# Kernel tuning notes

Hardware: AMD Instinct MI355X
Metric: run time of the kernel (lower is better)

The kernel has to match this reference:

```python
import jax, jax.numpy as jnp
import numpy as np

N = 50000
E = 800000


def gcn_conv(x, W, b, src, dst, norm):
    # x: [N, Fin] -> [N, Fout]; PyG GCNConv: linear, normalized scatter-add, bias
    h = x @ W                                  # [N, Fout]
    msg = h[src] * norm[:, None]               # [E+N, Fout] gather + scale
    out = jax.ops.segment_sum(msg, dst, num_segments=N)  # scatter-add
    return out + b


def _with_self_loops(edge_index):
    loops = jnp.arange(N, dtype=edge_index.dtype)
    src = jnp.concatenate([edge_index[0], loops])
    dst = jnp.concatenate([edge_index[1], loops])
    return src, dst


def _gcn_norm(src, dst):
    deg = jax.ops.segment_sum(jnp.ones_like(src, dtype=jnp.float32), dst, num_segments=N)
    dinv = jnp.where(deg > 0, jax.lax.rsqrt(jnp.maximum(deg, 1.0)), 0.0)
    return dinv[src] * dinv[dst]


def setup_inputs() -> dict:
    key = jax.random.key(0)
    ks = jax.random.split(key, 8)
    x = jax.random.normal(ks[0], (N, 128), dtype=jnp.float32)
    edge_index = jax.random.randint(ks[1], (2, E), 0, N, dtype=jnp.int64)
    # Glorot-ish init for the three GCNConv layers
    W1 = jax.random.normal(ks[2], (128, 64), dtype=jnp.float32) * (1.0 / np.sqrt(128))
    b1 = jnp.zeros((64,), dtype=jnp.float32)
    W2 = jax.random.normal(ks[3], (64, 64), dtype=jnp.float32) * (1.0 / np.sqrt(64))
    b2 = jnp.zeros((64,), dtype=jnp.float32)
    W3 = jax.random.normal(ks[4], (64, 40), dtype=jnp.float32) * (1.0 / np.sqrt(64))
    b3 = jnp.zeros((40,), dtype=jnp.float32)
    return {"x": x, "edge_index": edge_index, "W1": W1, "b1": b1,
            "W2": W2, "b2": b2, "W3": W3, "b3": b3}


def reference(x, edge_index, W1, b1, W2, b2, W3, b3):
    src, dst = _with_self_loops(edge_index)
    norm = _gcn_norm(src, dst)
    h = jax.nn.relu(gcn_conv(x, W1, b1, src, dst, norm))
    h = jax.nn.relu(gcn_conv(h, W2, b2, src, dst, norm))
    return gcn_conv(h, W3, b3, src, dst, norm)
```

## Files before the change

### kernel.cpp

```cpp
#include <hip/hip_runtime.h>

#define NNODE 50000
#define NEDGE 800000
#define NBUCKET 196
#define NPB 256
#define EPB 3125

typedef __attribute__((ext_vector_type(8))) unsigned short ushort8v;

__device__ inline unsigned short f2bf(float f) {
    unsigned int u = __float_as_uint(f);
    u += 0x7FFFu + ((u >> 16) & 1u);
    return (unsigned short)(u >> 16);
}
__device__ inline float bf2f(unsigned short h) {
    return __uint_as_float((unsigned int)h << 16);
}


__global__ __launch_bounds__(256) void k_histA(const int* __restrict__ dst, int* __restrict__ hist_g) {
    __shared__ int h[NBUCKET];
    const int tid = threadIdx.x, pb = blockIdx.x, e0 = pb * EPB;
    if (tid < NBUCKET) h[tid] = 0;
    __syncthreads();
    for (int i = tid; i < EPB; i += 256)
        atomicAdd(&h[dst[e0 + i] >> 8], 1);
    __syncthreads();
    if (tid < NBUCKET) hist_g[tid * 256 + pb] = h[tid];
}

__global__ __launch_bounds__(256) void k_scanA1(const int* __restrict__ hist_g, int* __restrict__ base_g,
                                                int* __restrict__ colsum) {
    __shared__ int s[256];
    const int b = blockIdx.x, t = threadIdx.x;
    int v = hist_g[b * 256 + t];
    s[t] = v;
    __syncthreads();
#pragma unroll
    for (int off = 1; off < 256; off <<= 1) {
        int a = (t >= off) ? s[t - off] : 0;
        __syncthreads();
        s[t] += a;
        __syncthreads();
    }
    base_g[b * 256 + t] = s[t] - v;
    if (t == 255) colsum[b] = s[t];
}

__device__ inline void scan_colsum(const int* __restrict__ colsum, int* cs, int tid) {
    cs[tid] = (tid < NBUCKET) ? colsum[tid] : 0;
    __syncthreads();
#pragma unroll
    for (int off = 1; off < 256; off <<= 1) {
        int a = (tid >= off) ? cs[tid - off] : 0;
        __syncthreads();
        cs[tid] += a;
        __syncthreads();
    }
}

__global__ __launch_bounds__(256) void k_scatterA(const int* __restrict__ src, const int* __restrict__ dst,
                          const int* __restrict__ base_g, const int* __restrict__ colsum,
                          unsigned int* __restrict__ bucketed) {
    __shared__ int cs[256];
    __shared__ int cur[NBUCKET];
    const int tid = threadIdx.x, pb = blockIdx.x, e0 = pb * EPB;
    scan_colsum(colsum, cs, tid);
    if (tid < NBUCKET) {
        int bb = (tid == 0) ? 0 : cs[tid - 1];
        cur[tid] = bb + base_g[tid * 256 + pb];
    }
    __syncthreads();
    for (int i = tid; i < EPB; i += 256) {
        int d = dst[e0 + i], s = src[e0 + i];
        int pos = atomicAdd(&cur[d >> 8], 1);
        bucketed[pos] = ((unsigned int)d << 16) | (unsigned int)s;
    }
}


__global__ __launch_bounds__(256) void k_bucketB2(const unsigned int* __restrict__ bucketed,
                          const int* __restrict__ colsum, int* __restrict__ rowstart,
                          unsigned short* __restrict__ csr_src, float* __restrict__ dinv) {
    __shared__ int cs[256];
    __shared__ int cnt[NPB];
    __shared__ int ex[NPB];
    __shared__ int cur[NPB];
    const int tid = threadIdx.x, b = blockIdx.x;
    scan_colsum(colsum, cs, tid);
    const int base_out = (b == 0) ? 0 : cs[b - 1];
    const int end_out  = cs[b];

    cnt[tid] = 0;
    __syncthreads();
    for (int i = base_out + tid; i < end_out; i += 256)
        atomicAdd(&cnt[(bucketed[i] >> 16) & 255], 1);
    __syncthreads();

    int v = cnt[tid];
    ex[tid] = v;
    __syncthreads();
#pragma unroll
    for (int off = 1; off < 256; off <<= 1) {
        int a = (tid >= off) ? ex[tid - off] : 0;
        __syncthreads();
        ex[tid] += a;
        __syncthreads();
    }
    int excl = ex[tid] - v;
    int node = (b << 8) + tid;
    cur[tid] = base_out + excl;
    if (node < NNODE) {
        rowstart[node] = base_out + excl;
        dinv[node] = rsqrtf((float)v + 1.0f);
    }
    if (b == 0 && tid == 0) rowstart[NNODE] = NEDGE;
    __syncthreads();

    for (int i = base_out + tid; i < end_out; i += 256) {
        unsigned int u = bucketed[i];
        int pos = atomicAdd(&cur[(u >> 16) & 255], 1);
        csr_src[pos] = (unsigned short)(u & 0xFFFFu);
    }
}


template<int FIN, int FOUT, typename XT>
__launch_bounds__(256)
__global__ void k_gemm_prescale(const XT* __restrict__ X, const float* __restrict__ W,
                                const float* __restrict__ dinv, unsigned short* __restrict__ XWs) {
    __shared__ float Xt[FIN * 68];
    __shared__ float Ws[FIN * 64];

    const int tid = threadIdx.x;
    const int r0 = blockIdx.x * 64;

    for (int idx = tid; idx < FIN * 64; idx += 256) {
        int k = idx >> 6, c = idx & 63;
        Ws[idx] = (c < FOUT) ? W[k * FOUT + c] : 0.0f;
    }

    if constexpr (sizeof(XT) == 4) {
        constexpr int CH = FIN / 4;
        constexpr int CSH = (FIN == 128) ? 5 : 4;
        for (int idx = tid; idx < 64 * CH; idx += 256) {
            int r_lo = idx & 7;
            int c = (idx >> 3) & (CH - 1);
            int r = ((idx >> (3 + CSH)) << 3) + r_lo;
            int rr = r0 + r; if (rr >= NNODE) rr = NNODE - 1;
            float4 v = *(const float4*)((const float*)X + (size_t)rr * FIN + c * 4);
            Xt[(4 * c + 0) * 68 + r] = v.x;
            Xt[(4 * c + 1) * 68 + r] = v.y;
            Xt[(4 * c + 2) * 68 + r] = v.z;
            Xt[(4 * c + 3) * 68 + r] = v.w;
        }
    } else {
        constexpr int CH = FIN / 8;
        constexpr int CSH = (FIN == 128) ? 4 : 3;
        for (int idx = tid; idx < 64 * CH; idx += 256) {
            int r_lo = idx & 7;
            int c = (idx >> 3) & (CH - 1);
            int r = ((idx >> (3 + CSH)) << 3) + r_lo;
            int rr = r0 + r; if (rr >= NNODE) rr = NNODE - 1;
            ushort8v v = *(const ushort8v*)((const unsigned short*)X + (size_t)rr * FIN + c * 8);
#pragma unroll
            for (int t = 0; t < 8; ++t)
                Xt[(8 * c + t) * 68 + r] = bf2f(v[t]);
        }
    }
    __syncthreads();

    const int cg = tid & 15;
    const int rg = tid >> 4;

    float acc[4][4] = {};
#pragma unroll 4
    for (int k = 0; k < FIN; ++k) {
        float4 xv = *(const float4*)&Xt[k * 68 + 4 * rg];
        float4 wv = *(const float4*)&Ws[k * 64 + 4 * cg];
#pragma unroll
        for (int i = 0; i < 4; ++i) {
            float xi = (i == 0) ? xv.x : (i == 1) ? xv.y : (i == 2) ? xv.z : xv.w;
            acc[i][0] = fmaf(xi, wv.x, acc[i][0]);
            acc[i][1] = fmaf(xi, wv.y, acc[i][1]);
            acc[i][2] = fmaf(xi, wv.z, acc[i][2]);
            acc[i][3] = fmaf(xi, wv.w, acc[i][3]);
        }
    }

    if (4 * cg + 4 <= FOUT) {
#pragma unroll
        for (int i = 0; i < 4; ++i) {
            int row = r0 + 4 * rg + i;
            if (row < NNODE) {
                float dv = dinv[row];
                ushort4 o = { f2bf(acc[i][0] * dv), f2bf(acc[i][1] * dv),
                              f2bf(acc[i][2] * dv), f2bf(acc[i][3] * dv) };
                *(ushort4*)(XWs + (size_t)row * FOUT + 4 * cg) = o;
            }
        }
    }
}


template<int F, bool RELU, bool OUTBF>
__launch_bounds__(256)
__global__ void k_aggregate(const unsigned short* __restrict__ XWs, const int* __restrict__ rowstart,
                            const unsigned short* __restrict__ csr_src, const float* __restrict__ dinv,
                            const float* __restrict__ b, void* __restrict__ outp) {
    constexpr int NQ = F / 8;
    const int wid  = threadIdx.x >> 6;
    const int lane = threadIdx.x & 63;
    const int g = lane >> 3;
    const int q = lane & 7;
    const int d = blockIdx.x * 4 + wid;
    if (d >= NNODE) return;

    const int beg = rowstart[d];
    const int end = rowstart[d + 1];
    const bool qa = (q < NQ);

    float acc[8] = {};

    for (int base = beg; base < end; base += 64) {
        int idx = base + lane;
        int sv = (idx < end) ? (int)csr_src[idx] : 0;
        int nv = min(64, end - base);
        for (int j = 0; j < nv; j += 8) {
            int jj = j + g;
            int s = __shfl(sv, jj);
            if (jj < nv && qa) {
                ushort8v v = *(const ushort8v*)(XWs + (size_t)s * F + 8 * q);
#pragma unroll
                for (int t = 0; t < 8; ++t) acc[t] += bf2f(v[t]);
            }
        }
    }

#pragma unroll
    for (int mask = 8; mask <= 32; mask <<= 1) {
#pragma unroll
        for (int t = 0; t < 8; ++t) acc[t] += __shfl_xor(acc[t], mask);
    }

    if (g == 0 && qa) {
        ushort8v self = *(const ushort8v*)(XWs + (size_t)d * F + 8 * q);
        float dv = dinv[d];
        float o[8];
#pragma unroll
        for (int t = 0; t < 8; ++t) {
            o[t] = fmaf(acc[t] + bf2f(self[t]), dv, b[8 * q + t]);
            if (RELU) o[t] = fmaxf(o[t], 0.f);
        }
        if (OUTBF) {
            ushort8v ov;
#pragma unroll
            for (int t = 0; t < 8; ++t) ov[t] = f2bf(o[t]);
            *(ushort8v*)((unsigned short*)outp + (size_t)d * F + 8 * q) = ov;
        } else {
            float4 o0 = { o[0], o[1], o[2], o[3] };
            float4 o1 = { o[4], o[5], o[6], o[7] };
            *(float4*)((float*)outp + (size_t)d * F + 8 * q)     = o0;
            *(float4*)((float*)outp + (size_t)d * F + 8 * q + 4) = o1;
        }
    }
}

extern "C" void kernel_launch(void* const* d_in, const int* in_sizes, int n_in,
                              void* d_out, int out_size, void* d_ws, size_t ws_size,
                              hipStream_t stream) {
    const float* x  = (const float*)d_in[0];
    const int*   ei = (const int*)d_in[1];
    const float* W1 = (const float*)d_in[2];
    const float* b1 = (const float*)d_in[3];
    const float* W2 = (const float*)d_in[4];
    const float* b2 = (const float*)d_in[5];
    const float* W3 = (const float*)d_in[6];
    const float* b3 = (const float*)d_in[7];
    float* out = (float*)d_out;

    const int* src = ei;
    const int* dst = ei + NEDGE;

    char* p = (char*)d_ws;
    auto alloc = [&](size_t bytes) { char* r = p; p += (bytes + 255) & ~size_t(255); return r; };
    unsigned int* bucketed = (unsigned int*)alloc((size_t)NEDGE * 4);
    int*   hist_g     = (int*)  alloc(NBUCKET * 256 * 4);
    int*   base_g     = (int*)  alloc(NBUCKET * 256 * 4);
    int*   colsum     = (int*)  alloc(NBUCKET * 4);
    int*   rowstart   = (int*)  alloc((NNODE + 1) * 4);
    unsigned short* csr_src = (unsigned short*)alloc((size_t)NEDGE * 2);
    float* dinv       = (float*)alloc(NNODE * 4);
    unsigned short* XWs = (unsigned short*)alloc((size_t)NNODE * 64 * 2 + 256);
    unsigned short* H1  = (unsigned short*)alloc((size_t)NNODE * 64 * 2 + 256);
    unsigned short* H2  = (unsigned short*)alloc((size_t)NNODE * 64 * 2 + 256);

    const int B = 256;
    const int gGemm = (NNODE + 63) / 64;
    const int gAgg  = (NNODE + 3) / 4;

    k_histA   <<<256, B, 0, stream>>>(dst, hist_g);
    k_scanA1  <<<NBUCKET, B, 0, stream>>>(hist_g, base_g, colsum);
    k_scatterA<<<256, B, 0, stream>>>(src, dst, base_g, colsum, bucketed);
    k_bucketB2<<<NBUCKET, B, 0, stream>>>(bucketed, colsum, rowstart, csr_src, dinv);

    k_gemm_prescale<128, 64, float><<<gGemm, B, 0, stream>>>(x, W1, dinv, XWs);
    k_aggregate<64, true, true><<<gAgg, B, 0, stream>>>(XWs, rowstart, csr_src, dinv, b1, H1);

    k_gemm_prescale<64, 64, unsigned short><<<gGemm, B, 0, stream>>>(H1, W2, dinv, XWs);
    k_aggregate<64, true, true><<<gAgg, B, 0, stream>>>(XWs, rowstart, csr_src, dinv, b2, H2);

    k_gemm_prescale<64, 40, unsigned short><<<gGemm, B, 0, stream>>>(H2, W3, dinv, XWs);
    k_aggregate<40, false, false><<<gAgg, B, 0, stream>>>(XWs, rowstart, csr_src, dinv, b3, out);
}
```

Baseline: 158.1 us.

## Fuse CSR build into one cooperative kernel with grid syncs; unpack bf16 via uint4

The four CSR-construction kernels (histogram, column scan, scatter into buckets, per-bucket sort) are merged into a single cooperative kernel. It runs on 242 blocks and uses grid.sync() between phases, removing three kernel launch boundaries. The chunk size changes so the edges fit in 242 blocks, and the scan now masks hist columns beyond CHUNKS. The aggregation kernel also loads neighbour rows as uint4 and unpacks bf16 pairs with shift/mask instead of a ushort8 vector. The cooperative launch requires all blocks to be co-resident, and grid syncs have their own cost.

```diff
diff --git a/kernel.cpp b/kernel.cpp
--- a/kernel.cpp
+++ b/kernel.cpp
@@ -1,10 +1,12 @@
 #include <hip/hip_runtime.h>
+#include <hip/hip_cooperative_groups.h>
 
 #define NNODE 50000
 #define NEDGE 800000
 #define NBUCKET 196
 #define NPB 256
-#define EPB 3125
+#define CHUNKS 242
+#define CEPB 3306
 
 typedef __attribute__((ext_vector_type(8))) unsigned short ushort8v;
 
@@ -16,111 +18,113 @@
 __device__ inline float bf2f(unsigned short h) {
     return __uint_as_float((unsigned int)h << 16);
 }
-
-
-__global__ __launch_bounds__(256) void k_histA(const int* __restrict__ dst, int* __restrict__ hist_g) {
-    __shared__ int h[NBUCKET];
-    const int tid = threadIdx.x, pb = blockIdx.x, e0 = pb * EPB;
-    if (tid < NBUCKET) h[tid] = 0;
-    __syncthreads();
-    for (int i = tid; i < EPB; i += 256)
-        atomicAdd(&h[dst[e0 + i] >> 8], 1);
-    __syncthreads();
-    if (tid < NBUCKET) hist_g[tid * 256 + pb] = h[tid];
-}
-
-__global__ __launch_bounds__(256) void k_scanA1(const int* __restrict__ hist_g, int* __restrict__ base_g,
-                                                int* __restrict__ colsum) {
-    __shared__ int s[256];
-    const int b = blockIdx.x, t = threadIdx.x;
-    int v = hist_g[b * 256 + t];
-    s[t] = v;
-    __syncthreads();
-#pragma unroll
-    for (int off = 1; off < 256; off <<= 1) {
-        int a = (t >= off) ? s[t - off] : 0;
-        __syncthreads();
-        s[t] += a;
-        __syncthreads();
-    }
-    base_g[b * 256 + t] = s[t] - v;
-    if (t == 255) colsum[b] = s[t];
-}
-
-__device__ inline void scan_colsum(const int* __restrict__ colsum, int* cs, int tid) {
-    cs[tid] = (tid < NBUCKET) ? colsum[tid] : 0;
-    __syncthreads();
-#pragma unroll
-    for (int off = 1; off < 256; off <<= 1) {
-        int a = (tid >= off) ? cs[tid - off] : 0;
-        __syncthreads();
-        cs[tid] += a;
-        __syncthreads();
-    }
-}
-
-__global__ __launch_bounds__(256) void k_scatterA(const int* __restrict__ src, const int* __restrict__ dst,
-                          const int* __restrict__ base_g, const int* __restrict__ colsum,
-                          unsigned int* __restrict__ bucketed) {
-    __shared__ int cs[256];
-    __shared__ int cur[NBUCKET];
-    const int tid = threadIdx.x, pb = blockIdx.x, e0 = pb * EPB;
-    scan_colsum(colsum, cs, tid);
-    if (tid < NBUCKET) {
-        int bb = (tid == 0) ? 0 : cs[tid - 1];
-        cur[tid] = bb + base_g[tid * 256 + pb];
-    }
-    __syncthreads();
-    for (int i = tid; i < EPB; i += 256) {
-        int d = dst[e0 + i], s = src[e0 + i];
-        int pos = atomicAdd(&cur[d >> 8], 1);
-        bucketed[pos] = ((unsigned int)d << 16) | (unsigned int)s;
-    }
-}
-
-
-__global__ __launch_bounds__(256) void k_bucketB2(const unsigned int* __restrict__ bucketed,
-                          const int* __restrict__ colsum, int* __restrict__ rowstart,
-                          unsigned short* __restrict__ csr_src, float* __restrict__ dinv) {
-    __shared__ int cs[256];
-    __shared__ int cnt[NPB];
-    __shared__ int ex[NPB];
-    __shared__ int cur[NPB];
-    const int tid = threadIdx.x, b = blockIdx.x;
-    scan_colsum(colsum, cs, tid);
-    const int base_out = (b == 0) ? 0 : cs[b - 1];
-    const int end_out  = cs[b];
-
-    cnt[tid] = 0;
-    __syncthreads();
-    for (int i = base_out + tid; i < end_out; i += 256)
-        atomicAdd(&cnt[(bucketed[i] >> 16) & 255], 1);
-    __syncthreads();
-
-    int v = cnt[tid];
-    ex[tid] = v;
-    __syncthreads();
-#pragma unroll
-    for (int off = 1; off < 256; off <<= 1) {
-        int a = (tid >= off) ? ex[tid - off] : 0;
-        __syncthreads();
-        ex[tid] += a;
-        __syncthreads();
-    }
-    int excl = ex[tid] - v;
-    int node = (b << 8) + tid;
-    cur[tid] = base_out + excl;
-    if (node < NNODE) {
-        rowstart[node] = base_out + excl;
-        dinv[node] = rsqrtf((float)v + 1.0f);
-    }
-    if (b == 0 && tid == 0) rowstart[NNODE] = NEDGE;
-    __syncthreads();
-
-    for (int i = base_out + tid; i < end_out; i += 256) {
-        unsigned int u = bucketed[i];
-        int pos = atomicAdd(&cur[(u >> 16) & 255], 1);
-        csr_src[pos] = (unsigned short)(u & 0xFFFFu);
+__device__ inline float bfLO(unsigned int u) { return __uint_as_float(u << 16); }
+__device__ inline float bfHI(unsigned int u) { return __uint_as_float(u & 0xFFFF0000u); }
+
+
+__global__ __launch_bounds__(256)
+void k_csr(const int* __restrict__ src, const int* __restrict__ dst,
+           int* __restrict__ hist_g, int* __restrict__ base_g, int* __restrict__ colsum,
+           unsigned int* __restrict__ bucketed, int* __restrict__ rowstart,
+           unsigned short* __restrict__ csr_src, float* __restrict__ dinv) {
+    cooperative_groups::grid_group grid = cooperative_groups::this_grid();
+    __shared__ int sA[256];
+    __shared__ int sB[256];
+    __shared__ int sC[256];
+    const int tid = threadIdx.x, bid = blockIdx.x;
+
+    {
+        const int e0 = bid * CEPB, e1 = min(e0 + CEPB, NEDGE);
+        if (tid < NBUCKET) sA[tid] = 0;
+        __syncthreads();
+        for (int i = e0 + tid; i < e1; i += 256) atomicAdd(&sA[dst[i] >> 8], 1);
+        __syncthreads();
+        if (tid < NBUCKET) hist_g[tid * 256 + bid] = sA[tid];
+    }
+    grid.sync();
+
+    if (bid < NBUCKET) {
+        int v = (tid < CHUNKS) ? hist_g[bid * 256 + tid] : 0;
+        sA[tid] = v;
+        __syncthreads();
+#pragma unroll
+        for (int off = 1; off < 256; off <<= 1) {
+            int a = (tid >= off) ? sA[tid - off] : 0;
+            __syncthreads();
+            sA[tid] += a;
+            __syncthreads();
+        }
+        base_g[bid * 256 + tid] = sA[tid] - v;
+        if (tid == 255) colsum[bid] = sA[255];
+    }
+    grid.sync();
+
+    {
+        sA[tid] = (tid < NBUCKET) ? colsum[tid] : 0;
+        __syncthreads();
+#pragma unroll
+        for (int off = 1; off < 256; off <<= 1) {
+            int a = (tid >= off) ? sA[tid - off] : 0;
+            __syncthreads();
+            sA[tid] += a;
+            __syncthreads();
+        }
+        if (tid < NBUCKET) {
+            int bb = (tid == 0) ? 0 : sA[tid - 1];
+            sB[tid] = bb + base_g[tid * 256 + bid];
+        }
+        __syncthreads();
+        const int e0 = bid * CEPB, e1 = min(e0 + CEPB, NEDGE);
+        for (int i = e0 + tid; i < e1; i += 256) {
+            int d = dst[i], s = src[i];
+            int pos = atomicAdd(&sB[d >> 8], 1);
+            bucketed[pos] = ((unsigned int)d << 16) | (unsigned int)s;
+        }
+    }
+    grid.sync();
+
+    if (bid < NBUCKET) {
+        sA[tid] = (tid < NBUCKET) ? colsum[tid] : 0;
+        __syncthreads();
+#pragma unroll
+        for (int off = 1; off < 256; off <<= 1) {
+            int a = (tid >= off) ? sA[tid - off] : 0;
+            __syncthreads();
+            sA[tid] += a;
+            __syncthreads();
+        }
+        const int base_out = (bid == 0) ? 0 : sA[bid - 1];
+        const int end_out  = sA[bid];
+        __syncthreads();
+        sB[tid] = 0;
+        __syncthreads();
+        for (int i = base_out + tid; i < end_out; i += 256)
+            atomicAdd(&sB[(bucketed[i] >> 16) & 255], 1);
+        __syncthreads();
+        int v = sB[tid];
+        sC[tid] = v;
+        __syncthreads();
+#pragma unroll
+        for (int off = 1; off < 256; off <<= 1) {
+            int a = (tid >= off) ? sC[tid - off] : 0;
+            __syncthreads();
+            sC[tid] += a;
+            __syncthreads();
+        }
+        int excl = sC[tid] - v;
+        int node = (bid << 8) + tid;
+        sB[tid] = base_out + excl;
+        if (node < NNODE) {
+            rowstart[node] = base_out + excl;
+            dinv[node] = rsqrtf((float)v + 1.0f);
+        }
+        if (bid == 0 && tid == 0) rowstart[NNODE] = NEDGE;
+        __syncthreads();
+        for (int i = base_out + tid; i < end_out; i += 256) {
+            unsigned int u = bucketed[i];
+            int pos = atomicAdd(&sB[(u >> 16) & 255], 1);
+            csr_src[pos] = (unsigned short)(u & 0xFFFFu);
+        }
     }
 }
 
@@ -230,9 +234,11 @@
             int jj = j + g;
             int s = __shfl(sv, jj);
             if (jj < nv && qa) {
-                ushort8v v = *(const ushort8v*)(XWs + (size_t)s * F + 8 * q);
-#pragma unroll
-                for (int t = 0; t < 8; ++t) acc[t] += bf2f(v[t]);
+                uint4 v = *(const uint4*)(XWs + (size_t)s * F + 8 * q);
+                acc[0] += bfLO(v.x); acc[1] += bfHI(v.x);
+                acc[2] += bfLO(v.y); acc[3] += bfHI(v.y);
+                acc[4] += bfLO(v.z); acc[5] += bfHI(v.z);
+                acc[6] += bfLO(v.w); acc[7] += bfHI(v.w);
             }
         }
     }
@@ -244,12 +250,14 @@
     }
 
     if (g == 0 && qa) {
-        ushort8v self = *(const ushort8v*)(XWs + (size_t)d * F + 8 * q);
+        uint4 sv4 = *(const uint4*)(XWs + (size_t)d * F + 8 * q);
+        float self[8] = { bfLO(sv4.x), bfHI(sv4.x), bfLO(sv4.y), bfHI(sv4.y),
+                          bfLO(sv4.z), bfHI(sv4.z), bfLO(sv4.w), bfHI(sv4.w) };
         float dv = dinv[d];
         float o[8];
 #pragma unroll
         for (int t = 0; t < 8; ++t) {
-            o[t] = fmaf(acc[t] + bf2f(self[t]), dv, b[8 * q + t]);
+            o[t] = fmaf(acc[t] + self[t], dv, b[8 * q + t]);
             if (RELU) o[t] = fmaxf(o[t], 0.f);
         }
         if (OUTBF) {
@@ -290,7 +298,7 @@
     int*   colsum     = (int*)  alloc(NBUCKET * 4);
     int*   rowstart   = (int*)  alloc((NNODE + 1) * 4);
     unsigned short* csr_src = (unsigned short*)alloc((size_t)NEDGE * 2);
-    float* dinv       = (float*)alloc(NNODE * 4);
+    float* dinvp      = (float*)alloc(NNODE * 4);
     unsigned short* XWs = (unsigned short*)alloc((size_t)NNODE * 64 * 2 + 256);
     unsigned short* H1  = (unsigned short*)alloc((size_t)NNODE * 64 * 2 + 256);
     unsigned short* H2  = (unsigned short*)alloc((size_t)NNODE * 64 * 2 + 256);
@@ -299,17 +307,17 @@
     const int gGemm = (NNODE + 63) / 64;
     const int gAgg  = (NNODE + 3) / 4;
 
-    k_histA   <<<256, B, 0, stream>>>(dst, hist_g);
-    k_scanA1  <<<NBUCKET, B, 0, stream>>>(hist_g, base_g, colsum);
-    k_scatterA<<<256, B, 0, stream>>>(src, dst, base_g, colsum, bucketed);
-    k_bucketB2<<<NBUCKET, B, 0, stream>>>(bucketed, colsum, rowstart, csr_src, dinv);
-
-    k_gemm_prescale<128, 64, float><<<gGemm, B, 0, stream>>>(x, W1, dinv, XWs);
-    k_aggregate<64, true, true><<<gAgg, B, 0, stream>>>(XWs, rowstart, csr_src, dinv, b1, H1);
-
-    k_gemm_prescale<64, 64, unsigned short><<<gGemm, B, 0, stream>>>(H1, W2, dinv, XWs);
-    k_aggregate<64, true, true><<<gAgg, B, 0, stream>>>(XWs, rowstart, csr_src, dinv, b2, H2);
-
-    k_gemm_prescale<64, 40, unsigned short><<<gGemm, B, 0, stream>>>(H2, W3, dinv, XWs);
-    k_aggregate<40, false, false><<<gAgg, B, 0, stream>>>(XWs, rowstart, csr_src, dinv, b3, out);
-}
+    void* args[] = { (void*)&src, (void*)&dst, (void*)&hist_g, (void*)&base_g,
+                     (void*)&colsum, (void*)&bucketed, (void*)&rowstart,
+                     (void*)&csr_src, (void*)&dinvp };
+    hipLaunchCooperativeKernel((const void*)k_csr, dim3(CHUNKS), dim3(B), args, 0, stream);
+
+    k_gemm_prescale<128, 64, float><<<gGemm, B, 0, stream>>>(x, W1, dinvp, XWs);
+    k_aggregate<64, true, true><<<gAgg, B, 0, stream>>>(XWs, rowstart, csr_src, dinvp, b1, H1);
+
+    k_gemm_prescale<64, 64, unsigned short><<<gGemm, B, 0, stream>>>(H1, W2, dinvp, XWs);
+    k_aggregate<64, true, true><<<gAgg, B, 0, stream>>>(XWs, rowstart, csr_src, dinvp, b2, H2);
+
+    k_gemm_prescale<64, 40, unsigned short><<<gGemm, B, 0, stream>>>(H2, W3, dinvp, XWs);
+    k_aggregate<40, false, false><<<gAgg, B, 0, stream>>>(XWs, rowstart, csr_src, dinvp, b3, out);
+}
```

Measured after the change: 259.1 us. 1.64x slower.

## Fuse aggregation with next layer's GEMM to skip hidden-state round trips

Applied to the files above, without the earlier changes.

Adds a k_agg_gemm kernel. Each block aggregates neighbor features for 64 nodes straight into shared memory, applies bias and ReLU, then multiplies by the next layer's weights and writes the dinv-prescaled bf16 result. This removes the bf16 H1/H2 global writes and reads and two kernel launches. As a side change, the bf16 unpack now reads uint4 and uses shift/mask helpers. The cost is that each block now runs the aggregation with only 4 wavefronts over 16 nodes each, with no gather overlap across separate kernels, which may lower parallelism in the latency-bound gather phase.

```diff
diff --git a/kernel.cpp b/kernel.cpp
--- a/kernel.cpp
+++ b/kernel.cpp
@@ -16,6 +16,8 @@
 __device__ inline float bf2f(unsigned short h) {
     return __uint_as_float((unsigned int)h << 16);
 }
+__device__ inline float bfLO(unsigned int u) { return __uint_as_float(u << 16); }
+__device__ inline float bfHI(unsigned int u) { return __uint_as_float(u & 0xFFFF0000u); }
 
 
 __global__ __launch_bounds__(256) void k_histA(const int* __restrict__ dst, int* __restrict__ hist_g) {
@@ -77,7 +79,6 @@
         bucketed[pos] = ((unsigned int)d << 16) | (unsigned int)s;
     }
 }
-
 
 __global__ __launch_bounds__(256) void k_bucketB2(const unsigned int* __restrict__ bucketed,
                           const int* __restrict__ colsum, int* __restrict__ rowstart,
@@ -125,9 +126,9 @@
 }
 
 
-template<int FIN, int FOUT, typename XT>
+template<int FIN, int FOUT>
 __launch_bounds__(256)
-__global__ void k_gemm_prescale(const XT* __restrict__ X, const float* __restrict__ W,
+__global__ void k_gemm_prescale(const float* __restrict__ X, const float* __restrict__ W,
                                 const float* __restrict__ dinv, unsigned short* __restrict__ XWs) {
     __shared__ float Xt[FIN * 68];
     __shared__ float Ws[FIN * 64];
@@ -140,33 +141,18 @@
         Ws[idx] = (c < FOUT) ? W[k * FOUT + c] : 0.0f;
     }
 
-    if constexpr (sizeof(XT) == 4) {
-        constexpr int CH = FIN / 4;
-        constexpr int CSH = (FIN == 128) ? 5 : 4;
-        for (int idx = tid; idx < 64 * CH; idx += 256) {
-            int r_lo = idx & 7;
-            int c = (idx >> 3) & (CH - 1);
-            int r = ((idx >> (3 + CSH)) << 3) + r_lo;
-            int rr = r0 + r; if (rr >= NNODE) rr = NNODE - 1;
-            float4 v = *(const float4*)((const float*)X + (size_t)rr * FIN + c * 4);
-            Xt[(4 * c + 0) * 68 + r] = v.x;
-            Xt[(4 * c + 1) * 68 + r] = v.y;
-            Xt[(4 * c + 2) * 68 + r] = v.z;
-            Xt[(4 * c + 3) * 68 + r] = v.w;
-        }
-    } else {
-        constexpr int CH = FIN / 8;
-        constexpr int CSH = (FIN == 128) ? 4 : 3;
-        for (int idx = tid; idx < 64 * CH; idx += 256) {
-            int r_lo = idx & 7;
-            int c = (idx >> 3) & (CH - 1);
-            int r = ((idx >> (3 + CSH)) << 3) + r_lo;
-            int rr = r0 + r; if (rr >= NNODE) rr = NNODE - 1;
-            ushort8v v = *(const ushort8v*)((const unsigned short*)X + (size_t)rr * FIN + c * 8);
-#pragma unroll
-            for (int t = 0; t < 8; ++t)
-                Xt[(8 * c + t) * 68 + r] = bf2f(v[t]);
-        }
+    constexpr int CH = FIN / 4;
+    constexpr int CSH = (FIN == 128) ? 5 : 4;
+    for (int idx = tid; idx < 64 * CH; idx += 256) {
+        int r_lo = idx & 7;
+        int c = (idx >> 3) & (CH - 1);
+        int r = ((idx >> (3 + CSH)) << 3) + r_lo;
+        int rr = r0 + r; if (rr >= NNODE) rr = NNODE - 1;
+        float4 v = *(const float4*)(X + (size_t)rr * FIN + c * 4);
+        Xt[(4 * c + 0) * 68 + r] = v.x;
+        Xt[(4 * c + 1) * 68 + r] = v.y;
+        Xt[(4 * c + 2) * 68 + r] = v.z;
+        Xt[(4 * c + 3) * 68 + r] = v.w;
     }
     __syncthreads();
 
@@ -203,11 +189,113 @@
 }
 
 
-template<int F, bool RELU, bool OUTBF>
+template<int FOUT>
+__launch_bounds__(256)
+__global__ void k_agg_gemm(const unsigned short* __restrict__ XWin, const int* __restrict__ rowstart,
+                           const unsigned short* __restrict__ csr_src, const float* __restrict__ dinv,
+                           const float* __restrict__ bias, const float* __restrict__ W,
+                           unsigned short* __restrict__ XWout) {
+    __shared__ float Xt[64 * 68];
+    __shared__ float Ws[64 * 64];
+
+    const int tid = threadIdx.x;
+    const int wid = tid >> 6, lane = tid & 63;
+    const int g = lane >> 3, q = lane & 7;
+    const int r0 = blockIdx.x * 64;
+
+    for (int idx = tid; idx < 64 * 64; idx += 256) {
+        int k = idx >> 6, c = idx & 63;
+        Ws[idx] = (c < FOUT) ? W[k * FOUT + c] : 0.0f;
+    }
+
+    float bb[8];
+#pragma unroll
+    for (int t = 0; t < 8; ++t) bb[t] = bias[8 * q + t];
+
+    for (int n = 0; n < 16; ++n) {
+        const int rr = wid * 16 + n;
+        const int d = r0 + rr;
+        if (d < NNODE) {
+            const int beg = rowstart[d];
+            const int end = rowstart[d + 1];
+            float acc[8] = {};
+            for (int base = beg; base < end; base += 64) {
+                int idx = base + lane;
+                int sv = (idx < end) ? (int)csr_src[idx] : 0;
+                int nv = min(64, end - base);
+                for (int j = 0; j < nv; j += 8) {
+                    int jj = j + g;
+                    int s = __shfl(sv, jj);
+                    if (jj < nv) {
+                        uint4 v = *(const uint4*)(XWin + (size_t)s * 64 + 8 * q);
+                        acc[0] += bfLO(v.x); acc[1] += bfHI(v.x);
+                        acc[2] += bfLO(v.y); acc[3] += bfHI(v.y);
+                        acc[4] += bfLO(v.z); acc[5] += bfHI(v.z);
+                        acc[6] += bfLO(v.w); acc[7] += bfHI(v.w);
+                    }
+                }
+            }
+#pragma unroll
+            for (int mask = 8; mask <= 32; mask <<= 1) {
+#pragma unroll
+                for (int t = 0; t < 8; ++t) acc[t] += __shfl_xor(acc[t], mask);
+            }
+            if (g == 0) {
+                uint4 sv4 = *(const uint4*)(XWin + (size_t)d * 64 + 8 * q);
+                float self[8] = { bfLO(sv4.x), bfHI(sv4.x), bfLO(sv4.y), bfHI(sv4.y),
+                                  bfLO(sv4.z), bfHI(sv4.z), bfLO(sv4.w), bfHI(sv4.w) };
+                float dv = dinv[d];
+#pragma unroll
+                for (int t = 0; t < 8; ++t) {
+                    float o = fmaf(acc[t] + self[t], dv, bb[t]);
+                    Xt[(8 * q + t) * 68 + rr] = fmaxf(o, 0.0f);
+                }
+            }
+        } else if (g == 0) {
+#pragma unroll
+            for (int t = 0; t < 8; ++t) Xt[(8 * q + t) * 68 + rr] = 0.0f;
+        }
+    }
+    __syncthreads();
+
+    const int cg = tid & 15;
+    const int rg = tid >> 4;
+
+    float acc[4][4] = {};
+#pragma unroll 4
+    for (int k = 0; k < 64; ++k) {
+        float4 xv = *(const float4*)&Xt[k * 68 + 4 * rg];
+        float4 wv = *(const float4*)&Ws[k * 64 + 4 * cg];
+#pragma unroll
+        for (int i = 0; i < 4; ++i) {
+            float xi = (i == 0) ? xv.x : (i == 1) ? xv.y : (i == 2) ? xv.z : xv.w;
+            acc[i][0] = fmaf(xi, wv.x, acc[i][0]);
+            acc[i][1] = fmaf(xi, wv.y, acc[i][1]);
+            acc[i][2] = fmaf(xi, wv.z, acc[i][2]);
+            acc[i][3] = fmaf(xi, wv.w, acc[i][3]);
+        }
+    }
+
+    if (4 * cg + 4 <= FOUT) {
+#pragma unroll
+        for (int i = 0; i < 4; ++i) {
+            int row = r0 + 4 * rg + i;
+            if (row < NNODE) {
+                float dv = dinv[row];
+                ushort4 o = { f2bf(acc[i][0] * dv), f2bf(acc[i][1] * dv),
+                              f2bf(acc[i][2] * dv), f2bf(acc[i][3] * dv) };
+                *(ushort4*)(XWout + (size_t)row * FOUT + 4 * cg) = o;
+            }
+        }
+    }
+}
+
+
+template<int F, bool RELU>
 __launch_bounds__(256)
 __global__ void k_aggregate(const unsigned short* __restrict__ XWs, const int* __restrict__ rowstart,
                             const unsigned short* __restrict__ csr_src, const float* __restrict__ dinv,
-                            const float* __restrict__ b, void* __restrict__ outp) {
+                            const float* __restrict__ b, float* __restrict__ out) {
     constexpr int NQ = F / 8;
     const int wid  = threadIdx.x >> 6;
     const int lane = threadIdx.x & 63;
@@ -230,9 +318,11 @@
             int jj = j + g;
             int s = __shfl(sv, jj);
             if (jj < nv && qa) {
-                ushort8v v = *(const ushort8v*)(XWs + (size_t)s * F + 8 * q);
-#pragma unroll
-                for (int t = 0; t < 8; ++t) acc[t] += bf2f(v[t]);
+                uint4 v = *(const uint4*)(XWs + (size_t)s * F + 8 * q);
+                acc[0] += bfLO(v.x); acc[1] += bfHI(v.x);
+                acc[2] += bfLO(v.y); acc[3] += bfHI(v.y);
+                acc[4] += bfLO(v.z); acc[5] += bfHI(v.z);
+                acc[6] += bfLO(v.w); acc[7] += bfHI(v.w);
             }
         }
     }
@@ -244,25 +334,20 @@
     }
 
     if (g == 0 && qa) {
-        ushort8v self = *(const ushort8v*)(XWs + (size_t)d * F + 8 * q);
+        uint4 sv4 = *(const uint4*)(XWs + (size_t)d * F + 8 * q);
+        float self[8] = { bfLO(sv4.x), bfHI(sv4.x), bfLO(sv4.y), bfHI(sv4.y),
+                          bfLO(sv4.z), bfHI(sv4.z), bfLO(sv4.w), bfHI(sv4.w) };
         float dv = dinv[d];
         float o[8];
 #pragma unroll
         for (int t = 0; t < 8; ++t) {
-            o[t] = fmaf(acc[t] + bf2f(self[t]), dv, b[8 * q + t]);
+            o[t] = fmaf(acc[t] + self[t], dv, b[8 * q + t]);
             if (RELU) o[t] = fmaxf(o[t], 0.f);
         }
-        if (OUTBF) {
-            ushort8v ov;
-#pragma unroll
-            for (int t = 0; t < 8; ++t) ov[t] = f2bf(o[t]);
-            *(ushort8v*)((unsigned short*)outp + (size_t)d * F + 8 * q) = ov;
-        } else {
-            float4 o0 = { o[0], o[1], o[2], o[3] };
-            float4 o1 = { o[4], o[5], o[6], o[7] };
-            *(float4*)((float*)outp + (size_t)d * F + 8 * q)     = o0;
-            *(float4*)((float*)outp + (size_t)d * F + 8 * q + 4) = o1;
-        }
+        float4 o0 = { o[0], o[1], o[2], o[3] };
+        float4 o1 = { o[4], o[5], o[6], o[7] };
+        *(float4*)(out + (size_t)d * F + 8 * q)     = o0;
+        *(float4*)(out + (size_t)d * F + 8 * q + 4) = o1;
     }
 }
 
@@ -290,10 +375,10 @@
     int*   colsum     = (int*)  alloc(NBUCKET * 4);
     int*   rowstart   = (int*)  alloc((NNODE + 1) * 4);
     unsigned short* csr_src = (unsigned short*)alloc((size_t)NEDGE * 2);
-    float* dinv       = (float*)alloc(NNODE * 4);
-    unsigned short* XWs = (unsigned short*)alloc((size_t)NNODE * 64 * 2 + 256);
-    unsigned short* H1  = (unsigned short*)alloc((size_t)NNODE * 64 * 2 + 256);
-    unsigned short* H2  = (unsigned short*)alloc((size_t)NNODE * 64 * 2 + 256);
+    float* dinvp      = (float*)alloc(NNODE * 4);
+    unsigned short* XWsA = (unsigned short*)alloc((size_t)NNODE * 64 * 2 + 256);
+    unsigned short* XWsB = (unsigned short*)alloc((size_t)NNODE * 64 * 2 + 256);
+    unsigned short* XWsC = (unsigned short*)alloc((size_t)NNODE * 40 * 2 + 256);
 
     const int B = 256;
     const int gGemm = (NNODE + 63) / 64;
@@ -302,14 +387,13 @@
     k_histA   <<<256, B, 0, stream>>>(dst, hist_g);
     k_scanA1  <<<NBUCKET, B, 0, stream>>>(hist_g, base_g, colsum);
     k_scatterA<<<256, B, 0, stream>>>(src, dst, base_g, colsum, bucketed);
-    k_bucketB2<<<NBUCKET, B, 0, stream>>>(bucketed, colsum, rowstart, csr_src, dinv);
-
-    k_gemm_prescale<128, 64, float><<<gGemm, B, 0, stream>>>(x, W1, dinv, XWs);
-    k_aggregate<64, true, true><<<gAgg, B, 0, stream>>>(XWs, rowstart, csr_src, dinv, b1, H1);
-
-    k_gemm_prescale<64, 64, unsigned short><<<gGemm, B, 0, stream>>>(H1, W2, dinv, XWs);
-    k_aggregate<64, true, true><<<gAgg, B, 0, stream>>>(XWs, rowstart, csr_src, dinv, b2, H2);
-
-    k_gemm_prescale<64, 40, unsigned short><<<gGemm, B, 0, stream>>>(H2, W3, dinv, XWs);
-    k_aggregate<40, false, false><<<gAgg, B, 0, stream>>>(XWs, rowstart, csr_src, dinv, b3, out);
-}
+    k_bucketB2<<<NBUCKET, B, 0, stream>>>(bucketed, colsum, rowstart, csr_src, dinvp);
+
+    k_gemm_prescale<128, 64><<<gGemm, B, 0, stream>>>(x, W1, dinvp, XWsA);
+
+    k_agg_gemm<64><<<gGemm, B, 0, stream>>>(XWsA, rowstart, csr_src, dinvp, b1, W2, XWsB);
+
+    k_agg_gemm<40><<<gGemm, B, 0, stream>>>(XWsB, rowstart, csr_src, dinvp, b2, W3, XWsC);
+
+    k_aggregate<40, false><<<gAgg, B, 0, stream>>>(XWsC, rowstart, csr_src, dinvp, b3, out);
+}
```

Result: slower. 179.2 us (+13.3%).

## Fuse layer-1 GEMM with histogram kernel and apply source dinv at aggregation

Applied to the files above, without the earlier changes.

The layer-1 X·W1 GEMM now runs in the same launch as the edge histogram, using extra blocks, so it no longer waits for the CSR build and dinv. Because dinv is not ready yet, the GEMM output is left unscaled, and the first aggregation multiplies each gathered neighbour row by dinv[src] through a new template flag. The aggregation inner loop is also unrolled two edges at a time and unpacks bf16 pairs from uint4 loads. In exchange, layer 1 does an extra dinv gather per edge, and the fused kernel reserves a large shared-memory footprint for the histogram blocks too.

```diff
diff --git a/kernel.cpp b/kernel.cpp
--- a/kernel.cpp
+++ b/kernel.cpp
@@ -5,6 +5,7 @@
 #define NBUCKET 196
 #define NPB 256
 #define EPB 3125
+#define G1BLK 782
 
 typedef __attribute__((ext_vector_type(8))) unsigned short ushort8v;
 
@@ -16,18 +17,76 @@
 __device__ inline float bf2f(unsigned short h) {
     return __uint_as_float((unsigned int)h << 16);
 }
-
-
-__global__ __launch_bounds__(256) void k_histA(const int* __restrict__ dst, int* __restrict__ hist_g) {
+__device__ inline float bfLO(unsigned int u) { return __uint_as_float(u << 16); }
+__device__ inline float bfHI(unsigned int u) { return __uint_as_float(u & 0xFFFF0000u); }
+
+
+__global__ __launch_bounds__(256)
+void k_hist_gemm1(const int* __restrict__ dst, int* __restrict__ hist_g,
+                  const float* __restrict__ x, const float* __restrict__ W1,
+                  unsigned short* __restrict__ XWs) {
+    __shared__ float Xt[128 * 68];
+    __shared__ float Ws[128 * 64];
     __shared__ int h[NBUCKET];
-    const int tid = threadIdx.x, pb = blockIdx.x, e0 = pb * EPB;
-    if (tid < NBUCKET) h[tid] = 0;
-    __syncthreads();
-    for (int i = tid; i < EPB; i += 256)
-        atomicAdd(&h[dst[e0 + i] >> 8], 1);
-    __syncthreads();
-    if (tid < NBUCKET) hist_g[tid * 256 + pb] = h[tid];
-}
+    const int tid = threadIdx.x, bid = blockIdx.x;
+
+    if (bid < 256) {
+        const int e0 = bid * EPB;
+        if (tid < NBUCKET) h[tid] = 0;
+        __syncthreads();
+        for (int i = tid; i < EPB; i += 256)
+            atomicAdd(&h[dst[e0 + i] >> 8], 1);
+        __syncthreads();
+        if (tid < NBUCKET) hist_g[tid * 256 + bid] = h[tid];
+        return;
+    }
+
+    const int r0 = (bid - 256) * 64;
+
+    for (int idx = tid; idx < 128 * 64; idx += 256)
+        Ws[idx] = W1[idx];
+
+    for (int idx = tid; idx < 64 * 32; idx += 256) {
+        int r_lo = idx & 7;
+        int c = (idx >> 3) & 31;
+        int r = ((idx >> 8) << 3) + r_lo;
+        int rr = r0 + r; if (rr >= NNODE) rr = NNODE - 1;
+        float4 v = *(const float4*)(x + (size_t)rr * 128 + c * 4);
+        Xt[(4 * c + 0) * 68 + r] = v.x;
+        Xt[(4 * c + 1) * 68 + r] = v.y;
+        Xt[(4 * c + 2) * 68 + r] = v.z;
+        Xt[(4 * c + 3) * 68 + r] = v.w;
+    }
+    __syncthreads();
+
+    const int cg = tid & 15;
+    const int rg = tid >> 4;
+
+    float acc[4][4] = {};
+#pragma unroll 4
+    for (int k = 0; k < 128; ++k) {
+        float4 xv = *(const float4*)&Xt[k * 68 + 4 * rg];
+        float4 wv = *(const float4*)&Ws[k * 64 + 4 * cg];
+#pragma unroll
+        for (int i = 0; i < 4; ++i) {
+            float xi = (i == 0) ? xv.x : (i == 1) ? xv.y : (i == 2) ? xv.z : xv.w;
+            acc[i][0] = fmaf(xi, wv.x, acc[i][0]);
+            acc[i][1] = fmaf(xi, wv.y, acc[i][1]);
+            acc[i][2] = fmaf(xi, wv.z, acc[i][2]);
+            acc[i][3] = fmaf(xi, wv.w, acc[i][3]);
+        }
+    }
+
+#pragma unroll
+    for (int i = 0; i < 4; ++i) {
+        int row = r0 + 4 * rg + i;
+        if (row < NNODE) {
+            ushort4 o = { f2bf(acc[i][0]), f2bf(acc[i][1]), f2bf(acc[i][2]), f2bf(acc[i][3]) };
+            *(ushort4*)(XWs + (size_t)row * 64 + 4 * cg) = o;
+        }
+    }
+}
+
 
 __global__ __launch_bounds__(256) void k_scanA1(const int* __restrict__ hist_g, int* __restrict__ base_g,
                                                 int* __restrict__ colsum) {
@@ -77,7 +136,6 @@
         bucketed[pos] = ((unsigned int)d << 16) | (unsigned int)s;
     }
 }
-
 
 __global__ __launch_bounds__(256) void k_bucketB2(const unsigned int* __restrict__ bucketed,
                           const int* __restrict__ colsum, int* __restrict__ rowstart,
@@ -125,9 +183,9 @@
 }
 
 
-template<int FIN, int FOUT, typename XT>
+template<int FIN, int FOUT>
 __launch_bounds__(256)
-__global__ void k_gemm_prescale(const XT* __restrict__ X, const float* __restrict__ W,
+__global__ void k_gemm_prescale(const unsigned short* __restrict__ X, const float* __restrict__ W,
                                 const float* __restrict__ dinv, unsigned short* __restrict__ XWs) {
     __shared__ float Xt[FIN * 68];
     __shared__ float Ws[FIN * 64];
@@ -140,33 +198,17 @@
         Ws[idx] = (c < FOUT) ? W[k * FOUT + c] : 0.0f;
     }
 
-    if constexpr (sizeof(XT) == 4) {
-        constexpr int CH = FIN / 4;
-        constexpr int CSH = (FIN == 128) ? 5 : 4;
-        for (int idx = tid; idx < 64 * CH; idx += 256) {
-            int r_lo = idx & 7;
-            int c = (idx >> 3) & (CH - 1);
-            int r = ((idx >> (3 + CSH)) << 3) + r_lo;
-            int rr = r0 + r; if (rr >= NNODE) rr = NNODE - 1;
-            float4 v = *(const float4*)((const float*)X + (size_t)rr * FIN + c * 4);
-            Xt[(4 * c + 0) * 68 + r] = v.x;
-            Xt[(4 * c + 1) * 68 + r] = v.y;
-            Xt[(4 * c + 2) * 68 + r] = v.z;
-            Xt[(4 * c + 3) * 68 + r] = v.w;
-        }
-    } else {
-        constexpr int CH = FIN / 8;
-        constexpr int CSH = (FIN == 128) ? 4 : 3;
-        for (int idx = tid; idx < 64 * CH; idx += 256) {
-            int r_lo = idx & 7;
-            int c = (idx >> 3) & (CH - 1);
-            int r = ((idx >> (3 + CSH)) << 3) + r_lo;
-            int rr = r0 + r; if (rr >= NNODE) rr = NNODE - 1;
-            ushort8v v = *(const ushort8v*)((const unsigned short*)X + (size_t)rr * FIN + c * 8);
-#pragma unroll
-            for (int t = 0; t < 8; ++t)
-                Xt[(8 * c + t) * 68 + r] = bf2f(v[t]);
-        }
+    constexpr int CH = FIN / 8;
+    constexpr int CSH = (FIN == 128) ? 4 : 3;
+    for (int idx = tid; idx < 64 * CH; idx += 256) {
+        int r_lo = idx & 7;
+        int c = (idx >> 3) & (CH - 1);
+        int r = ((idx >> (3 + CSH)) << 3) + r_lo;
+        int rr = r0 + r; if (rr >= NNODE) rr = NNODE - 1;
+        ushort8v v = *(const ushort8v*)(X + (size_t)rr * FIN + c * 8);
+#pragma unroll
+        for (int t = 0; t < 8; ++t)
+            Xt[(8 * c + t) * 68 + r] = bf2f(v[t]);
     }
     __syncthreads();
 
@@ -203,7 +245,7 @@
 }
 
 
-template<int F, bool RELU, bool OUTBF>
+template<int F, bool RELU, bool OUTBF, bool EDGE_DINV>
 __launch_bounds__(256)
 __global__ void k_aggregate(const unsigned short* __restrict__ XWs, const int* __restrict__ rowstart,
                             const unsigned short* __restrict__ csr_src, const float* __restrict__ dinv,
@@ -226,13 +268,73 @@
         int idx = base + lane;
         int sv = (idx < end) ? (int)csr_src[idx] : 0;
         int nv = min(64, end - base);
-        for (int j = 0; j < nv; j += 8) {
-            int jj = j + g;
+        int nf = nv >> 3;
+        int k = 0;
+        for (; k + 2 <= nf; k += 2) {
+            int sA = __shfl(sv, 8 * k + g);
+            int sB = __shfl(sv, 8 * k + 8 + g);
+            if (qa) {
+                uint4 vA = *(const uint4*)(XWs + (size_t)sA * F + 8 * q);
+                uint4 vB = *(const uint4*)(XWs + (size_t)sB * F + 8 * q);
+                float dA = EDGE_DINV ? dinv[sA] : 1.0f;
+                float dB = EDGE_DINV ? dinv[sB] : 1.0f;
+                if (EDGE_DINV) {
+                    acc[0] = fmaf(bfLO(vA.x), dA, acc[0]); acc[1] = fmaf(bfHI(vA.x), dA, acc[1]);
+                    acc[2] = fmaf(bfLO(vA.y), dA, acc[2]); acc[3] = fmaf(bfHI(vA.y), dA, acc[3]);
+                    acc[4] = fmaf(bfLO(vA.z), dA, acc[4]); acc[5] = fmaf(bfHI(vA.z), dA, acc[5]);
+                    acc[6] = fmaf(bfLO(vA.w), dA, acc[6]); acc[7] = fmaf(bfHI(vA.w), dA, acc[7]);
+                    acc[0] = fmaf(bfLO(vB.x), dB, acc[0]); acc[1] = fmaf(bfHI(vB.x), dB, acc[1]);
+                    acc[2] = fmaf(bfLO(vB.y), dB, acc[2]); acc[3] = fmaf(bfHI(vB.y), dB, acc[3]);
+                    acc[4] = fmaf(bfLO(vB.z), dB, acc[4]); acc[5] = fmaf(bfHI(vB.z), dB, acc[5]);
+                    acc[6] = fmaf(bfLO(vB.w), dB, acc[6]); acc[7] = fmaf(bfHI(vB.w), dB, acc[7]);
+                } else {
+                    acc[0] += bfLO(vA.x); acc[1] += bfHI(vA.x);
+                    acc[2] += bfLO(vA.y); acc[3] += bfHI(vA.y);
+                    acc[4] += bfLO(vA.z); acc[5] += bfHI(vA.z);
+                    acc[6] += bfLO(vA.w); acc[7] += bfHI(vA.w);
+                    acc[0] += bfLO(vB.x); acc[1] += bfHI(vB.x);
+                    acc[2] += bfLO(vB.y); acc[3] += bfHI(vB.y);
+                    acc[4] += bfLO(vB.z); acc[5] += bfHI(vB.z);
+                    acc[6] += bfLO(vB.w); acc[7] += bfHI(vB.w);
+                }
+            }
+        }
+        for (; k < nf; ++k) {
+            int s = __shfl(sv, 8 * k + g);
+            if (qa) {
+                uint4 v = *(const uint4*)(XWs + (size_t)s * F + 8 * q);
+                float ds = EDGE_DINV ? dinv[s] : 1.0f;
+                if (EDGE_DINV) {
+                    acc[0] = fmaf(bfLO(v.x), ds, acc[0]); acc[1] = fmaf(bfHI(v.x), ds, acc[1]);
+                    acc[2] = fmaf(bfLO(v.y), ds, acc[2]); acc[3] = fmaf(bfHI(v.y), ds, acc[3]);
+                    acc[4] = fmaf(bfLO(v.z), ds, acc[4]); acc[5] = fmaf(bfHI(v.z), ds, acc[5]);
+                    acc[6] = fmaf(bfLO(v.w), ds, acc[6]); acc[7] = fmaf(bfHI(v.w), ds, acc[7]);
+                } else {
+                    acc[0] += bfLO(v.x); acc[1] += bfHI(v.x);
+                    acc[2] += bfLO(v.y); acc[3] += bfHI(v.y);
+                    acc[4] += bfLO(v.z); acc[5] += bfHI(v.z);
+                    acc[6] += bfLO(v.w); acc[7] += bfHI(v.w);
+                }
+            }
+        }
+        int rem = nv - (nf << 3);
+        if (rem) {
+            int jj = (nf << 3) + g;
             int s = __shfl(sv, jj);
-            if (jj < nv && qa) {
-                ushort8v v = *(const ushort8v*)(XWs + (size_t)s * F + 8 * q);
-#pragma unroll
-                for (int t = 0; t < 8; ++t) acc[t] += bf2f(v[t]);
+            if (g < rem && qa) {
+                uint4 v = *(const uint4*)(XWs + (size_t)s * F + 8 * q);
+                float ds = EDGE_DINV ? dinv[s] : 1.0f;
+                if (EDGE_DINV) {
+                    acc[0] = fmaf(bfLO(v.x), ds, acc[0]); acc[1] = fmaf(bfHI(v.x), ds, acc[1]);
+                    acc[2] = fmaf(bfLO(v.y), ds, acc[2]); acc[3] = fmaf(bfHI(v.y), ds, acc[3]);
+                    acc[4] = fmaf(bfLO(v.z), ds, acc[4]); acc[5] = fmaf(bfHI(v.z), ds, acc[5]);
+                    acc[6] = fmaf(bfLO(v.w), ds, acc[6]); acc[7] = fmaf(bfHI(v.w), ds, acc[7]);
+                } else {
+                    acc[0] += bfLO(v.x); acc[1] += bfHI(v.x);
+                    acc[2] += bfLO(v.y); acc[3] += bfHI(v.y);
+                    acc[4] += bfLO(v.z); acc[5] += bfHI(v.z);
+                    acc[6] += bfLO(v.w); acc[7] += bfHI(v.w);
+                }
             }
         }
     }
@@ -244,12 +346,15 @@
     }
 
     if (g == 0 && qa) {
-        ushort8v self = *(const ushort8v*)(XWs + (size_t)d * F + 8 * q);
+        uint4 sv4 = *(const uint4*)(XWs + (size_t)d * F + 8 * q);
+        float self[8] = { bfLO(sv4.x), bfHI(sv4.x), bfLO(sv4.y), bfHI(sv4.y),
+                          bfLO(sv4.z), bfHI(sv4.z), bfLO(sv4.w), bfHI(sv4.w) };
         float dv = dinv[d];
+        float ss = EDGE_DINV ? dv : 1.0f;
         float o[8];
 #pragma unroll
         for (int t = 0; t < 8; ++t) {
-            o[t] = fmaf(acc[t] + bf2f(self[t]), dv, b[8 * q + t]);
+            o[t] = fmaf(acc[t] + self[t] * ss, dv, b[8 * q + t]);
             if (RELU) o[t] = fmaxf(o[t], 0.f);
         }
         if (OUTBF) {
@@ -290,7 +395,7 @@
     int*   colsum     = (int*)  alloc(NBUCKET * 4);
     int*   rowstart   = (int*)  alloc((NNODE + 1) * 4);
     unsigned short* csr_src = (unsigned short*)alloc((size_t)NEDGE * 2);
-    float* dinv       = (float*)alloc(NNODE * 4);
+    float* dinvp      = (float*)alloc(NNODE * 4);
     unsigned short* XWs = (unsigned short*)alloc((size_t)NNODE * 64 * 2 + 256);
     unsigned short* H1  = (unsigned short*)alloc((size_t)NNODE * 64 * 2 + 256);
     unsigned short* H2  = (unsigned short*)alloc((size_t)NNODE * 64 * 2 + 256);
@@ -299,17 +404,16 @@
     const int gGemm = (NNODE + 63) / 64;
     const int gAgg  = (NNODE + 3) / 4;
 
-    k_histA   <<<256, B, 0, stream>>>(dst, hist_g);
+    k_hist_gemm1<<<256 + G1BLK, B, 0, stream>>>(dst, hist_g, x, W1, XWs);
     k_scanA1  <<<NBUCKET, B, 0, stream>>>(hist_g, base_g, colsum);
     k_scatterA<<<256, B, 0, stream>>>(src, dst, base_g, colsum, bucketed);
-    k_bucketB2<<<NBUCKET, B, 0, stream>>>(bucketed, colsum, rowstart, csr_src, dinv);
-
-    k_gemm_prescale<128, 64, float><<<gGemm, B, 0, stream>>>(x, W1, dinv, XWs);
-    k_aggregate<64, true, true><<<gAgg, B, 0, stream>>>(XWs, rowstart, csr_src, dinv, b1, H1);
-
-    k_gemm_prescale<64, 64, unsigned short><<<gGemm, B, 0, stream>>>(H1, W2, dinv, XWs);
-    k_aggregate<64, true, true><<<gAgg, B, 0, stream>>>(XWs, rowstart, csr_src, dinv, b2, H2);
-
-    k_gemm_prescale<64, 40, unsigned short><<<gGemm, B, 0, stream>>>(H2, W3, dinv, XWs);
-    k_aggregate<40, false, false><<<gAgg, B, 0, stream>>>(XWs, rowstart, csr_src, dinv, b3, out);
-}
+    k_bucketB2<<<NBUCKET, B, 0, stream>>>(bucketed, colsum, rowstart, csr_src, dinvp);
+
+    k_aggregate<64, true, true, true><<<gAgg, B, 0, stream>>>(XWs, rowstart, csr_src, dinvp, b1, H1);
+
+    k_gemm_prescale<64, 64><<<gGemm, B, 0, stream>>>(H1, W2, dinvp, XWs);
+    k_aggregate<64, true, true, false><<<gAgg, B, 0, stream>>>(XWs, rowstart, csr_src, dinvp, b2, H2);
+
+    k_gemm_prescale<64, 40><<<gGemm, B, 0, stream>>>(H2, W3, dinvp, XWs);
+    k_aggregate<40, false, false, false><<<gAgg, B, 0, stream>>>(XWs, rowstart, csr_src, dinvp, b3, out);
+}
```

Result: faster. 150.3 us (median of 2 runs) (-4.9%).
